# Performance work log

Hardware: AMD Instinct MI355X
Metric: run time of the kernel (lower is better)

The kernel has to match this reference:

```python
import jax, jax.numpy as jnp
import numpy as np

H, DH = 6, 64
D = H * DH
SQRT_DH = np.float32(np.sqrt(DH))


def _pool_norm(tok, ids):
    # masked mean pooling over tokens, then L2 normalize (Encoder.mean_pooling + normalize)
    mask = (ids > 0).astype(tok.dtype)[:, :, None]
    s = jnp.sum(tok * mask, axis=1) / jnp.clip(jnp.sum(mask, axis=1), 1e-9, None)
    return s / jnp.clip(jnp.linalg.norm(s, axis=1, keepdims=True), 1e-12, None)


def setup_inputs() -> dict:
    key = jax.random.key(0)
    ks = jax.random.split(key, 16)
    N_MSG, N_CON, L, E = 10000, 20000, 16, 128000
    s = 0.05
    eye = jnp.eye(DH, dtype=jnp.float32)
    inp = {}
    inp['tok_msg'] = jax.random.normal(ks[0], (N_MSG, L, D), jnp.float32)
    inp['tok_con'] = jax.random.normal(ks[1], (N_CON, L, D), jnp.float32)
    inp['ids_msg'] = jax.random.randint(ks[2], (N_MSG, L), 0, 100)
    inp['ids_con'] = jax.random.randint(ks[3], (N_CON, L), 0, 100)
    inp['src_cm'] = jax.random.randint(ks[4], (E,), 0, N_CON)
    inp['dst_cm'] = jax.random.randint(ks[5], (E,), 0, N_MSG)
    inp['src_mc'] = jax.random.randint(ks[6], (E,), 0, N_MSG)
    inp['dst_mc'] = jax.random.randint(ks[7], (E,), 0, N_CON)
    inp['lin_W'] = jax.random.normal(ks[8], (2, D, D), jnp.float32) * s
    inp['lin_b'] = jnp.zeros((2, D), jnp.float32)
    inp['kW'] = jax.random.normal(ks[9], (2, 2, D, D), jnp.float32) * s
    inp['kb'] = jnp.zeros((2, 2, D), jnp.float32)
    inp['qW'] = jax.random.normal(ks[10], (2, 2, D, D), jnp.float32) * s
    inp['qb'] = jnp.zeros((2, 2, D), jnp.float32)
    inp['vW'] = jax.random.normal(ks[11], (2, 2, D, D), jnp.float32) * s
    inp['vb'] = jnp.zeros((2, 2, D), jnp.float32)
    inp['aW'] = jax.random.normal(ks[12], (2, 2, D, D), jnp.float32) * s
    inp['ab'] = jnp.zeros((2, 2, D), jnp.float32)
    inp['a_rel'] = jax.random.normal(ks[13], (2, 2, H, DH, DH), jnp.float32) * s + eye
    inp['m_rel'] = jax.random.normal(ks[14], (2, 2, H, DH, DH), jnp.float32) * s + eye
    inp['p_rel'] = jnp.ones((2, 2, H), jnp.float32)
    inp['skip'] = jnp.ones((2, 2), jnp.float32)
    return inp


def _hgt_layer(xs, edges, kW, kb, qW, qb, vW, vb, aW, ab, a_rel, m_rel, p_rel, skip):
    # xs = [x_message, x_concept]; edges = ((src, dst) per edge type)
    k = [(xs[t] @ kW[t] + kb[t]).reshape(-1, H, DH) for t in (0, 1)]
    q = [(xs[t] @ qW[t] + qb[t]).reshape(-1, H, DH) for t in (0, 1)]
    v = [(xs[t] @ vW[t] + vb[t]).reshape(-1, H, DH) for t in (0, 1)]
    edge_meta = ((1, 0), (0, 1))  # edge type e -> (src_type, dst_type)
    agg = [None, None]
    for e, (s, d) in enumerate(edge_meta):
        si, di = edges[e]
        Nd = xs[d].shape[0]
        # relation-specific key/message transforms, per head: [E, H, DH]
        ke = jnp.einsum('ehd,hdf->ehf', k[s][si], a_rel[e])
        score = jnp.einsum('ehf,ehf->eh', q[d][di], ke) * p_rel[e] / SQRT_DH
        # softmax over incoming edges per destination node
        m = jax.ops.segment_max(score, di, num_segments=Nd)
        ex = jnp.exp(score - m[di])
        den = jax.ops.segment_sum(ex, di, num_segments=Nd)
        alpha = ex / den[di]
        msg = jnp.einsum('ehd,hdf->ehf', v[s][si], m_rel[e]) * alpha[:, :, None]
        agg[d] = jax.ops.segment_sum(msg, di, num_segments=Nd).reshape(Nd, D)
    out = []
    for t in (0, 1):
        o = jax.nn.gelu(agg[t], approximate=False) @ aW[t] + ab[t]
        a = jax.nn.sigmoid(skip[t])
        out.append(a * o + (1.0 - a) * xs[t])
    return out


def reference(tok_msg, tok_con, ids_msg, ids_con, src_cm, dst_cm, src_mc, dst_mc,
              lin_W, lin_b, kW, kb, qW, qb, vW, vb, aW, ab, a_rel, m_rel, p_rel, skip):
    x0 = jax.nn.relu(_pool_norm(tok_msg, ids_msg) @ lin_W[0] + lin_b[0])
    x1 = jax.nn.relu(_pool_norm(tok_con, ids_con) @ lin_W[1] + lin_b[1])
    edges = ((src_cm, dst_cm), (src_mc, dst_mc))
    xs = [x0, x1]
    for l in range(2):  # num_layers = 2 (hard-coded in MedicalEncoder)
        xs = _hgt_layer(xs, edges, kW[l], kb[l], qW[l], qb[l], vW[l], vb[l],
                        aW[l], ab[l], a_rel[l], m_rel[l], p_rel[l], skip[l])
    return xs[0]  # x_dict['message']
```

## Files before the change

kernel.cpp:

```cpp
#include <hip/hip_runtime.h>
#include <math.h>

#define H 6
#define DH 64
#define D 384
#define L 16
#define WSZ ((size_t)(D) * (D))
#define RSZ ((size_t)(H) * (DH) * (DH))

typedef __attribute__((ext_vector_type(8))) short short8;
typedef __attribute__((ext_vector_type(4))) float f32x4;
typedef unsigned int uint_;

__device__ __forceinline__ float bf2f(unsigned short u) {
  union { unsigned int i; float f; } x; x.i = ((unsigned int)u) << 16; return x.f;
}
__device__ __forceinline__ unsigned short f2bf(float f) {
  unsigned int x = __float_as_uint(f);
  x = x + 0x7fffu + ((x >> 16) & 1u);
  return (unsigned short)(x >> 16);
}
__device__ __forceinline__ float blo(unsigned int u) { return __uint_as_float(u << 16); }
__device__ __forceinline__ float bhi(unsigned int u) { return __uint_as_float(u & 0xffff0000u); }
__device__ __forceinline__ float geluf(float x) {
  return 0.5f * x * (1.0f + erff(x * 0.70710678118654752f));
}

__global__ void zero_int_kernel(int* p, long n) {
  long i = (long)blockIdx.x * blockDim.x + threadIdx.x;
  long stride = (long)gridDim.x * blockDim.x;
  for (; i < n; i += stride) p[i] = 0;
}

__global__ void pool_norm_kernel(const float* __restrict__ tokM, const int* __restrict__ idsM,
                                 unsigned short* __restrict__ outM, int NM,
                                 const float* __restrict__ tokC, const int* __restrict__ idsC,
                                 unsigned short* __restrict__ outC) {
  int n = blockIdx.x;
  const float* tok; const int* ids; unsigned short* out;
  if (n < NM) { tok = tokM; ids = idsM; out = outM; }
  else { n -= NM; tok = tokC; ids = idsC; out = outC; }
  int t = threadIdx.x;
  int rg = t / 96, c4 = t % 96;
  const float4* tp = (const float4*)(tok + (size_t)n * L * D);
  const int* ip = ids + (size_t)n * L;
  int cnt = 0;
#pragma unroll
  for (int l = 0; l < L; ++l) cnt += (ip[l] > 0);
  float4 s = {0.f, 0.f, 0.f, 0.f};
#pragma unroll
  for (int li = 0; li < 4; ++li) {
    int l = rg + li * 4;
    if (ip[l] > 0) {
      float4 v = tp[l * 96 + c4];
      s.x += v.x; s.y += v.y; s.z += v.z; s.w += v.w;
    }
  }
  __shared__ float4 part[4][96];
  part[rg][c4] = s;
  __syncthreads();
  float4 m4 = {0.f, 0.f, 0.f, 0.f};
  float dot = 0.f;
  float inv_cnt = 1.0f / fmaxf((float)cnt, 1e-9f);
  if (t < 96) {
    float4 a = part[0][t], b = part[1][t], c = part[2][t], d2 = part[3][t];
    m4.x = (a.x + b.x + c.x + d2.x) * inv_cnt;
    m4.y = (a.y + b.y + c.y + d2.y) * inv_cnt;
    m4.z = (a.z + b.z + c.z + d2.z) * inv_cnt;
    m4.w = (a.w + b.w + c.w + d2.w) * inv_cnt;
    dot = m4.x * m4.x + m4.y * m4.y + m4.z * m4.z + m4.w * m4.w;
  }
#pragma unroll
  for (int o = 32; o; o >>= 1) dot += __shfl_down(dot, o);
  __shared__ float wpart[6];
  if ((t & 63) == 0) wpart[t >> 6] = dot;
  __syncthreads();
  float tot = 0.f;
#pragma unroll
  for (int i = 0; i < 6; ++i) tot += wpart[i];
  float inv = 1.0f / fmaxf(sqrtf(tot), 1e-12f);
  if (t < 96) {
    uint2 o;
    o.x = (uint_)f2bf(m4.x * inv) | ((uint_)f2bf(m4.y * inv) << 16);
    o.y = (uint_)f2bf(m4.z * inv) | ((uint_)f2bf(m4.w * inv) << 16);
    ((uint2*)(out + (size_t)n * D))[t] = o;
  }
}

__global__ void prepw_kernel(const float* __restrict__ lin_W, const float* __restrict__ kW,
                             const float* __restrict__ qW, const float* __restrict__ vW,
                             const float* __restrict__ aW, const float* __restrict__ a_rel,
                             const float* __restrict__ m_rel, const float* __restrict__ p_rel,
                             const float* __restrict__ kb, const float* __restrict__ qb,
                             const float* __restrict__ vb,
                             unsigned short* __restrict__ wbuf, float* __restrict__ bbuf) {
  int z = blockIdx.z;
  int tx = threadIdx.x, ty = threadIdx.y;
  if (z == 14) {
    int i = (blockIdx.y * 12 + blockIdx.x) * 1024 + ty * 32 + tx;
    if (i >= 3456) return;
    int gemm, col;
    if (i < 1152) { gemm = 0; col = i; }
    else if (i < 2304) { gemm = 1; col = i - 1152; }
    else if (i < 2688) { gemm = 2; col = i - 2304; }
    else { gemm = 3; col = i - 2688; }
    int sec = col / D, j = col % D, h = j >> 6, r = j & 63;
    float out = 0.f;
    if (gemm == 0) {
      if (sec == 0) out = kb[j];
      else if (sec == 1) {
        const float* R = a_rel + (size_t)h * 4096 + (size_t)r * 64;
        float s = 0.f; for (int f = 0; f < 64; ++f) s += qb[h * 64 + f] * R[f];
        out = s * p_rel[h] * 0.125f;
      } else {
        const float* Mm = m_rel + RSZ + (size_t)h * 4096;
        float s = 0.f; for (int d = 0; d < 64; ++d) s += vb[h * 64 + d] * Mm[d * 64 + r]; out = s;
      }
    } else if (gemm == 1) {
      if (sec == 0) out = kb[D + j];
      else if (sec == 1) {
        const float* R = a_rel + RSZ + (size_t)h * 4096 + (size_t)r * 64;
        float s = 0.f; for (int f = 0; f < 64; ++f) s += qb[D + h * 64 + f] * R[f];
        out = s * p_rel[H + h] * 0.125f;
      } else {
        const float* Mm = m_rel + (size_t)h * 4096;
        float s = 0.f; for (int d = 0; d < 64; ++d) s += vb[D + h * 64 + d] * Mm[d * 64 + r]; out = s;
      }
    } else if (gemm == 2) {
      const float* R = a_rel + 2 * RSZ + (size_t)h * 4096 + (size_t)r * 64;
      float s = 0.f; for (int f = 0; f < 64; ++f) s += qb[2 * D + h * 64 + f] * R[f];
      out = s * p_rel[2 * H + h] * 0.125f;
    } else {
      if (sec == 0) out = kb[3 * D + j];
      else {
        const float* Mm = m_rel + 2 * RSZ + (size_t)h * 4096;
        float s = 0.f; for (int d = 0; d < 64; ++d) s += vb[3 * D + h * 64 + d] * Mm[d * 64 + r]; out = s;
      }
    }
    bbuf[i] = out;
    return;
  }
  const float* src; const float* rel = nullptr; const float* prl = nullptr; int type = 0;
  switch (z) {
    case 0: src = lin_W; break;
    case 1: src = lin_W + WSZ; break;
    case 2: src = kW; break;
    case 3: type = 1; src = qW; rel = a_rel; prl = p_rel; break;
    case 4: type = 2; src = vW; rel = m_rel + RSZ; break;
    case 5: src = kW + WSZ; break;
    case 6: type = 1; src = qW + WSZ; rel = a_rel + RSZ; prl = p_rel + H; break;
    case 7: type = 2; src = vW + WSZ; rel = m_rel; break;
    case 8: type = 1; src = qW + 2 * WSZ; rel = a_rel + 2 * RSZ; prl = p_rel + 2 * H; break;
    case 9: src = kW + 3 * WSZ; break;
    case 10: type = 2; src = vW + 3 * WSZ; rel = m_rel + 2 * RSZ; break;
    case 11: src = aW; break;
    case 12: src = aW + WSZ; break;
    default: src = aW + 2 * WSZ; break;
  }
  unsigned short* dst = wbuf + (size_t)z * WSZ;
  int bx = blockIdx.x * 32;
  int by = blockIdx.y * 32;
  if (type == 0) {
    __shared__ float tile[32][33];
    tile[ty][tx] = src[(size_t)(bx + ty) * D + by + tx];
    __syncthreads();
    dst[(size_t)(by + ty) * D + bx + tx] = f2bf(tile[tx][ty]);
  } else if (type == 1) {
    int h = by >> 6, d0 = by & 63;
    float sc = prl[h] * 0.125f;
    __shared__ float Wt_[32][65], Rt[32][65];
#pragma unroll
    for (int half = 0; half < 2; ++half) {
      Wt_[ty][tx + half * 32] = src[(size_t)(bx + ty) * D + h * 64 + tx + half * 32];
      Rt[ty][tx + half * 32] = rel[(size_t)h * 4096 + (size_t)(d0 + ty) * 64 + tx + half * 32];
    }
    __syncthreads();
    float s = 0.f;
#pragma unroll 16
    for (int f = 0; f < 64; ++f) s += Wt_[tx][f] * Rt[ty][f];
    dst[(size_t)(by + ty) * D + bx + tx] = f2bf(s * sc);
  } else {
    int h = by >> 6, f0 = by & 63;
    __shared__ float Wt_[32][65];
    __shared__ float Mt[64][33];
#pragma unroll
    for (int half = 0; half < 2; ++half) {
      Wt_[ty][tx + half * 32] = src[(size_t)(bx + ty) * D + h * 64 + tx + half * 32];
      Mt[ty * 2 + half][tx] = rel[(size_t)h * 4096 + (size_t)(ty * 2 + half) * 64 + f0 + tx];
    }
    __syncthreads();
    float s = 0.f;
#pragma unroll 16
    for (int d = 0; d < 64; ++d) s += Wt_[tx][d] * Mt[d][ty];
    dst[(size_t)(by + ty) * D + bx + tx] = f2bf(s);
  }
}

__global__ void count2_kernel(const int* __restrict__ d0, const int* __restrict__ d1,
                              int* __restrict__ deg0, int* __restrict__ deg1, int E) {
  int e = blockIdx.x * blockDim.x + threadIdx.x;
  if (e < E) atomicAdd(&deg0[d0[e]], 1);
  else if (e < 2 * E) atomicAdd(&deg1[d1[e - E]], 1);
}

__global__ void scan2_kernel(const int* __restrict__ deg0, int* __restrict__ off0, int N0,
                             const int* __restrict__ deg1, int* __restrict__ off1, int N1) {
  const int* deg = blockIdx.x ? deg1 : deg0;
  int* off = blockIdx.x ? off1 : off0;
  int N = blockIdx.x ? N1 : N0;
  __shared__ int wsum[16];
  __shared__ int carrySh;
  int tid = threadIdx.x;
  int lane = tid & 63, wid = tid >> 6;
  if (tid == 0) carrySh = 0;
  __syncthreads();
  for (int base = 0; base < N; base += 1024) {
    int i = base + tid;
    int v = (i < N) ? deg[i] : 0;
    int s = v;
#pragma unroll
    for (int o = 1; o < 64; o <<= 1) {
      int t = __shfl_up(s, o);
      if (lane >= o) s += t;
    }
    if (lane == 63) wsum[wid] = s;
    __syncthreads();
    int wpre = 0;
    for (int j = 0; j < wid; ++j) wpre += wsum[j];
    int c = carrySh;
    if (i < N) off[i] = c + wpre + s - v;
    __syncthreads();
    if (tid == 1023) carrySh = c + wpre + s;
    __syncthreads();
  }
  if (tid == 0) off[N] = carrySh;
}

__global__ void scatter2_kernel(const int* __restrict__ d0, const int* __restrict__ s0,
                                const int* __restrict__ off0, int* __restrict__ cur0,
                                int* __restrict__ el0,
                                const int* __restrict__ d1, const int* __restrict__ s1,
                                const int* __restrict__ off1, int* __restrict__ cur1,
                                int* __restrict__ el1, int E) {
  int e = blockIdx.x * blockDim.x + threadIdx.x;
  if (e < E) {
    int d = d0[e];
    el0[off0[d] + atomicAdd(&cur0[d], 1)] = s0[e];
  } else if (e < 2 * E) {
    int ee = e - E;
    int d = d1[ee];
    el1[off1[d] + atomicAdd(&cur1[d], 1)] = s1[ee];
  }
}

struct AttnP {
  const unsigned short* kb;
  const unsigned short* tqb;
  const unsigned short* vmb;
  const int* off;
  const int* elist;
  unsigned short* aggb;
  int N, sk, st, sv, nb;
};

__global__ void attn_kernel(AttnP a0, AttnP a1) {
  bool first = (int)blockIdx.x < a0.nb;
  AttnP a = first ? a0 : a1;
  int bx = first ? (int)blockIdx.x : (int)blockIdx.x - a0.nb;
  int node = bx * 4 + (threadIdx.x >> 6);
  int lane = threadIdx.x & 63;
  if (node >= a.N) return;
  int e0 = a.off[node], e1 = a.off[node + 1];
  const uint_* tq32 = (const uint_*)(a.tqb + (size_t)node * a.st);
  float tq0[3], tq1[3], m[3], den[3], ac0[3], ac1[3];
#pragma unroll
  for (int j = 0; j < 3; ++j) {
    uint_ u = tq32[lane + 64 * j];
    tq0[j] = blo(u); tq1[j] = bhi(u);
    m[j] = -1e30f; den[j] = 0.f; ac0[j] = 0.f; ac1[j] = 0.f;
  }
  int i = e0;
  for (; i + 2 <= e1; i += 2) {
    int s0 = a.elist[i], s1 = a.elist[i + 1];
    const uint_* k0 = (const uint_*)(a.kb + (size_t)s0 * a.sk);
    const uint_* k1 = (const uint_*)(a.kb + (size_t)s1 * a.sk);
    const uint_* v0 = (const uint_*)(a.vmb + (size_t)s0 * a.sv);
    const uint_* v1 = (const uint_*)(a.vmb + (size_t)s1 * a.sv);
    float pa[3], pb[3]; uint_ va[3], vb[3];
#pragma unroll
    for (int j = 0; j < 3; ++j) {
      uint_ ka = k0[lane + 64 * j], kbu = k1[lane + 64 * j];
      va[j] = v0[lane + 64 * j]; vb[j] = v1[lane + 64 * j];
      pa[j] = blo(ka) * tq0[j] + bhi(ka) * tq1[j];
      pb[j] = blo(kbu) * tq0[j] + bhi(kbu) * tq1[j];
    }
#pragma unroll
    for (int o = 1; o <= 16; o <<= 1)
#pragma unroll
      for (int j = 0; j < 3; ++j) {
        pa[j] += __shfl_xor(pa[j], o);
        pb[j] += __shfl_xor(pb[j], o);
      }
#pragma unroll
    for (int j = 0; j < 3; ++j) {
      float mn = fmaxf(m[j], fmaxf(pa[j], pb[j]));
      float r = __expf(m[j] - mn);
      float p0 = __expf(pa[j] - mn);
      float p1 = __expf(pb[j] - mn);
      den[j] = den[j] * r + p0 + p1;
      ac0[j] = ac0[j] * r + p0 * blo(va[j]) + p1 * blo(vb[j]);
      ac1[j] = ac1[j] * r + p0 * bhi(va[j]) + p1 * bhi(vb[j]);
      m[j] = mn;
    }
  }
  if (i < e1) {
    int s0 = a.elist[i];
    const uint_* k0 = (const uint_*)(a.kb + (size_t)s0 * a.sk);
    const uint_* v0 = (const uint_*)(a.vmb + (size_t)s0 * a.sv);
    float pa[3]; uint_ va[3];
#pragma unroll
    for (int j = 0; j < 3; ++j) {
      uint_ ka = k0[lane + 64 * j];
      va[j] = v0[lane + 64 * j];
      pa[j] = blo(ka) * tq0[j] + bhi(ka) * tq1[j];
    }
#pragma unroll
    for (int o = 1; o <= 16; o <<= 1)
#pragma unroll
      for (int j = 0; j < 3; ++j) pa[j] += __shfl_xor(pa[j], o);
#pragma unroll
    for (int j = 0; j < 3; ++j) {
      float mn = fmaxf(m[j], pa[j]);
      float r = __expf(m[j] - mn);
      float p0 = __expf(pa[j] - mn);
      den[j] = den[j] * r + p0;
      ac0[j] = ac0[j] * r + p0 * blo(va[j]);
      ac1[j] = ac1[j] * r + p0 * bhi(va[j]);
      m[j] = mn;
    }
  }
  uint_* op32 = (uint_*)(a.aggb + (size_t)node * D);
#pragma unroll
  for (int j = 0; j < 3; ++j) {
    float o0 = (e1 > e0) ? ac0[j] / den[j] : 0.f;
    float o1 = (e1 > e0) ? ac1[j] / den[j] : 0.f;
    op32[lane + 64 * j] = (uint_)f2bf(geluf(o0)) | ((uint_)f2bf(geluf(o1)) << 16);
  }
}

struct GemmP {
  const unsigned short* A;
  const unsigned short* Wt;
  const float* bias;
  float* Cf;
  unsigned short* Cb;
  const float* xold;
  const float* skipPtr;
  int M, N, cpitch, relu;
};

__global__ __launch_bounds__(256) void gemm_bf16(GemmP q0, GemmP q1) {
  GemmP p = blockIdx.z ? q1 : q0;
  const int bm = blockIdx.x * 128, bn = blockIdx.y * 128;
  if (bm >= p.M || bn >= p.N) return;
  __shared__ __align__(16) unsigned short As[2][128 * 64];
  __shared__ __align__(16) unsigned short Bs[2][128 * 64];
  const int tid = threadIdx.x;
  const int w = tid >> 6, lane = tid & 63;

  auto stage = [&](int t, int buf) {
#pragma unroll
    for (int i = 0; i < 4; ++i) {
      int cid = (w * 4 + i) * 64 + lane;
      int row = cid >> 3;
      int cg = (cid & 7) ^ (row & 7);
      int grow = bm + row;
      if (grow >= p.M) grow = p.M - 1;
      const unsigned short* gp = p.A + (size_t)grow * D + t * 64 + cg * 8;
      __builtin_amdgcn_global_load_lds((const __attribute__((address_space(1))) void*)gp,
                                       (__attribute__((address_space(3))) void*)&As[buf][(w * 4 + i) * 512],
                                       16, 0, 0);
    }
#pragma unroll
    for (int i = 0; i < 4; ++i) {
      int cid = (w * 4 + i) * 64 + lane;
      int row = cid >> 3;
      int cg = (cid & 7) ^ (row & 7);
      const unsigned short* gp = p.Wt + (size_t)(bn + row) * D + t * 64 + cg * 8;
      __builtin_amdgcn_global_load_lds((const __attribute__((address_space(1))) void*)gp,
                                       (__attribute__((address_space(3))) void*)&Bs[buf][(w * 4 + i) * 512],
                                       16, 0, 0);
    }
  };

  stage(0, 0);
  __syncthreads();

  const int wr = w >> 1, wc = w & 1;
  const int la = lane & 15, hi = lane >> 4;
  f32x4 acc[4][4] = {};

  for (int t = 0; t < 6; ++t) {
    if (t < 5) stage(t + 1, (t + 1) & 1);
    const unsigned short* Ab = As[t & 1];
    const unsigned short* Bb = Bs[t & 1];
#pragma unroll
    for (int ks = 0; ks < 2; ++ks) {
      int c = ks * 4 + hi;
      short8 af[4], bfr[4];
#pragma unroll
      for (int mi = 0; mi < 4; ++mi) {
        int row = wr * 64 + mi * 16 + la;
        af[mi] = *(const short8*)&Ab[row * 64 + ((c ^ (row & 7)) * 8)];
      }
#pragma unroll
      for (int n = 0; n < 4; ++n) {
        int col = wc * 64 + n * 16 + la;
        bfr[n] = *(const short8*)&Bb[col * 64 + ((c ^ (col & 7)) * 8)];
      }
#pragma unroll
      for (int mi = 0; mi < 4; ++mi)
#pragma unroll
        for (int n = 0; n < 4; ++n)
          acc[mi][n] = __builtin_amdgcn_mfma_f32_16x16x32_bf16(af[mi], bfr[n], acc[mi][n], 0, 0, 0);
    }
    __syncthreads();
  }

  float sa = 0.f;
  if (p.xold) sa = 1.0f / (1.0f + __expf(-*p.skipPtr));
#pragma unroll
  for (int mi = 0; mi < 4; ++mi) {
#pragma unroll
    for (int n = 0; n < 4; ++n) {
#pragma unroll
      for (int r = 0; r < 4; ++r) {
        int row = bm + wr * 64 + mi * 16 + hi * 4 + r;
        int col = bn + wc * 64 + n * 16 + la;
        if (row >= p.M) continue;
        float v = acc[mi][n][r] + p.bias[col];
        if (p.relu) v = fmaxf(v, 0.f);
        if (p.xold) v = sa * v + (1.0f - sa) * p.xold[(size_t)row * D + col];
        if (p.Cf) p.Cf[(size_t)row * p.cpitch + col] = v;
        if (p.Cb) p.Cb[(size_t)row * p.cpitch + col] = f2bf(v);
      }
    }
  }
}

extern "C" void kernel_launch(void* const* d_in, const int* in_sizes, int n_in,
                              void* d_out, int out_size, void* d_ws, size_t ws_size,
                              hipStream_t stream) {
  const float* tok_msg = (const float*)d_in[0];
  const float* tok_con = (const float*)d_in[1];
  const int* ids_msg = (const int*)d_in[2];
  const int* ids_con = (const int*)d_in[3];
  const int* src_cm = (const int*)d_in[4];
  const int* dst_cm = (const int*)d_in[5];
  const int* src_mc = (const int*)d_in[6];
  const int* dst_mc = (const int*)d_in[7];
  const float* lin_W = (const float*)d_in[8];
  const float* lin_b = (const float*)d_in[9];
  const float* kW = (const float*)d_in[10];
  const float* kb = (const float*)d_in[11];
  const float* qW = (const float*)d_in[12];
  const float* qb = (const float*)d_in[13];
  const float* vW = (const float*)d_in[14];
  const float* vb = (const float*)d_in[15];
  const float* aW = (const float*)d_in[16];
  const float* ab = (const float*)d_in[17];
  const float* a_rel = (const float*)d_in[18];
  const float* m_rel = (const float*)d_in[19];
  const float* p_rel = (const float*)d_in[20];
  const float* skip = (const float*)d_in[21];

  const int NM = in_sizes[2] / L;
  const int NC = in_sizes[3] / L;
  const int E = in_sizes[4];

  char* wsb = (char*)d_ws;
  size_t woff = 0;
  auto alloc = [&](size_t bytes) {
    woff = (woff + 255) & ~(size_t)255;
    void* p = wsb + woff;
    woff += bytes;
    return p;
  };
  const size_t NMe = (size_t)NM * D, NCe = (size_t)NC * D;
  unsigned short* poolM = (unsigned short*)alloc(NMe * 2);
  unsigned short* poolC = (unsigned short*)alloc(NCe * 2);
  float* x0f = (float*)alloc(NMe * 4);
  float* x1f = (float*)alloc(NCe * 4);
  float* xn0f = (float*)alloc(NMe * 4);
  unsigned short* x0b = (unsigned short*)alloc(NMe * 2);
  unsigned short* x1b = (unsigned short*)alloc(NCe * 2);
  unsigned short* xn0b = (unsigned short*)alloc(NMe * 2);
  unsigned short* xn1b = (unsigned short*)alloc(NCe * 2);
  unsigned short* projM1 = (unsigned short*)alloc((size_t)NM * 1152 * 2);
  unsigned short* projC1 = (unsigned short*)alloc((size_t)NC * 1152 * 2);
  unsigned short* projM2 = (unsigned short*)alloc((size_t)NM * 384 * 2);
  unsigned short* projC2 = (unsigned short*)alloc((size_t)NC * 768 * 2);
  unsigned short* aggM = (unsigned short*)alloc(NMe * 2);
  unsigned short* aggC = (unsigned short*)alloc(NCe * 2);
  unsigned short* wbuf = (unsigned short*)alloc(14 * WSZ * 2);
  float* bbuf = (float*)alloc(3456 * 4);
  long nz = 2L * NM + 2L * NC;
  int* ibase = (int*)alloc((size_t)(nz + NM + 1 + NC + 1 + 2L * E) * 4);
  int* deg0 = ibase;
  int* cur0 = deg0 + NM;
  int* deg1 = cur0 + NM;
  int* cur1 = deg1 + NC;
  int* off0 = cur1 + NC;
  int* off1 = off0 + NM + 1;
  int* el0 = off1 + NC + 1;
  int* el1 = el0 + E;

  dim3 b256(256);
  const int mbM = (NM + 127) / 128, mbC = (NC + 127) / 128;
  const int mbMax = (mbM > mbC) ? mbM : mbC;

  prepw_kernel<<<dim3(12, 12, 15), dim3(32, 32), 0, stream>>>(lin_W, kW, qW, vW, aW, a_rel,
                                                              m_rel, p_rel, kb, qb, vb, wbuf, bbuf);

  zero_int_kernel<<<64, b256, 0, stream>>>(ibase, nz);
  int eg2 = (2 * E + 255) / 256;
  count2_kernel<<<eg2, b256, 0, stream>>>(dst_cm, dst_mc, deg0, deg1, E);
  scan2_kernel<<<2, 1024, 0, stream>>>(deg0, off0, NM, deg1, off1, NC);
  scatter2_kernel<<<eg2, b256, 0, stream>>>(dst_cm, src_cm, off0, cur0, el0,
                                            dst_mc, src_mc, off1, cur1, el1, E);

  pool_norm_kernel<<<NM + NC, D, 0, stream>>>(tok_msg, ids_msg, poolM, NM, tok_con, ids_con, poolC);

  {
    GemmP p0 = {poolM, wbuf, lin_b, x0f, x0b, nullptr, nullptr, NM, D, D, 1};
    GemmP p1 = {poolC, wbuf + WSZ, lin_b + D, x1f, x1b, nullptr, nullptr, NC, D, D, 1};
    gemm_bf16<<<dim3(mbMax, 3, 2), b256, 0, stream>>>(p0, p1);
  }
  {
    GemmP p0 = {x0b, wbuf + 2 * WSZ, bbuf, nullptr, projM1, nullptr, nullptr, NM, 1152, 1152, 0};
    GemmP p1 = {x1b, wbuf + 5 * WSZ, bbuf + 1152, nullptr, projC1, nullptr, nullptr, NC, 1152, 1152, 0};
    gemm_bf16<<<dim3(mbMax, 9, 2), b256, 0, stream>>>(p0, p1);
  }
  {
    AttnP a0 = {projC1, projM1 + 384, projC1 + 768, off0, el0, aggM, NM, 1152, 1152, 1152, (NM + 3) / 4};
    AttnP a1 = {projM1, projC1 + 384, projM1 + 768, off1, el1, aggC, NC, 1152, 1152, 1152, (NC + 3) / 4};
    attn_kernel<<<(NM + 3) / 4 + (NC + 3) / 4, b256, 0, stream>>>(a0, a1);
  }
  {
    GemmP p0 = {aggM, wbuf + 11 * WSZ, ab, xn0f, xn0b, x0f, skip + 0, NM, D, D, 0};
    GemmP p1 = {aggC, wbuf + 12 * WSZ, ab + D, nullptr, xn1b, x1f, skip + 1, NC, D, D, 0};
    gemm_bf16<<<dim3(mbMax, 3, 2), b256, 0, stream>>>(p0, p1);
  }
  {
    GemmP p0 = {xn0b, wbuf + 8 * WSZ, bbuf + 2304, nullptr, projM2, nullptr, nullptr, NM, 384, 384, 0};
    GemmP p1 = {xn1b, wbuf + 9 * WSZ, bbuf + 2688, nullptr, projC2, nullptr, nullptr, NC, 768, 768, 0};
    gemm_bf16<<<dim3(mbMax, 6, 2), b256, 0, stream>>>(p0, p1);
  }
  {
    AttnP a0 = {projC2, projM2, projC2 + 384, off0, el0, aggM, NM, 768, 384, 768, (NM + 3) / 4};
    AttnP a1 = a0;
    attn_kernel<<<(NM + 3) / 4, b256, 0, stream>>>(a0, a1);
  }
  {
    GemmP p0 = {aggM, wbuf + 13 * WSZ, ab + 2 * D, (float*)d_out, nullptr, xn0f, skip + 2, NM, D, D, 0};
    GemmP p1 = p0;
    gemm_bf16<<<dim3(mbM, 3, 1), b256, 0, stream>>>(p0, p1);
  }
}
```

Baseline: 686.6 us.

## Fuse graph CSR build into pool, prep and GEMM kernels; drop fp32 residual copies

Edge degree counting now runs inside the pooling kernel, and the prefix scan is merged with the weight-prep kernel. The CSR scatter runs as an extra z-slice of the first GEMM launch. Together these cut several small kernel launches and let the graph preprocessing overlap with real work. The fp32 copies of the residual activations are removed and the skip connection reads the bf16 copies instead, which reduces memory traffic but lowers residual precision.

```diff
diff --git a/kernel.cpp b/kernel.cpp
--- a/kernel.cpp
+++ b/kernel.cpp
@@ -32,10 +32,20 @@
   for (; i < n; i += stride) p[i] = 0;
 }
 
-__global__ void pool_norm_kernel(const float* __restrict__ tokM, const int* __restrict__ idsM,
-                                 unsigned short* __restrict__ outM, int NM,
-                                 const float* __restrict__ tokC, const int* __restrict__ idsC,
-                                 unsigned short* __restrict__ outC) {
+__global__ void pool_count_kernel(const float* __restrict__ tokM, const int* __restrict__ idsM,
+                                  unsigned short* __restrict__ outM, int NM,
+                                  const float* __restrict__ tokC, const int* __restrict__ idsC,
+                                  unsigned short* __restrict__ outC,
+                                  const int* __restrict__ dc0, const int* __restrict__ dc1,
+                                  int* __restrict__ deg0, int* __restrict__ deg1, int E, int CH) {
+  {
+    int base = blockIdx.x * CH;
+    int e = base + threadIdx.x;
+    if (threadIdx.x < CH && e < 2 * E) {
+      if (e < E) atomicAdd(&deg0[dc0[e]], 1);
+      else atomicAdd(&deg1[dc1[e - E]], 1);
+    }
+  }
   int n = blockIdx.x;
   const float* tok; const int* ids; unsigned short* out;
   if (n < NM) { tok = tokM; ids = idsM; out = outM; }
@@ -87,54 +97,92 @@
   }
 }
 
-__global__ void prepw_kernel(const float* __restrict__ lin_W, const float* __restrict__ kW,
-                             const float* __restrict__ qW, const float* __restrict__ vW,
-                             const float* __restrict__ aW, const float* __restrict__ a_rel,
-                             const float* __restrict__ m_rel, const float* __restrict__ p_rel,
-                             const float* __restrict__ kb, const float* __restrict__ qb,
-                             const float* __restrict__ vb,
-                             unsigned short* __restrict__ wbuf, float* __restrict__ bbuf) {
-  int z = blockIdx.z;
-  int tx = threadIdx.x, ty = threadIdx.y;
+__global__ void prepscan_kernel(const float* __restrict__ lin_W, const float* __restrict__ kW,
+                                const float* __restrict__ qW, const float* __restrict__ vW,
+                                const float* __restrict__ aW, const float* __restrict__ a_rel,
+                                const float* __restrict__ m_rel, const float* __restrict__ p_rel,
+                                const float* __restrict__ kb, const float* __restrict__ qb,
+                                const float* __restrict__ vb,
+                                unsigned short* __restrict__ wbuf, float* __restrict__ bbuf,
+                                const int* __restrict__ deg0, int* __restrict__ off0, int N0,
+                                const int* __restrict__ deg1, int* __restrict__ off1, int N1) {
+  int bxg = blockIdx.x;
+  int tid = threadIdx.x;
+  if (bxg < 2) {
+    const int* deg = bxg ? deg1 : deg0;
+    int* off = bxg ? off1 : off0;
+    int N = bxg ? N1 : N0;
+    __shared__ int wsum[16];
+    __shared__ int carrySh;
+    int lane = tid & 63, wid = tid >> 6;
+    if (tid == 0) carrySh = 0;
+    __syncthreads();
+    for (int base = 0; base < N; base += 1024) {
+      int i = base + tid;
+      int v = (i < N) ? deg[i] : 0;
+      int s = v;
+#pragma unroll
+      for (int o = 1; o < 64; o <<= 1) {
+        int t2 = __shfl_up(s, o);
+        if (lane >= o) s += t2;
+      }
+      if (lane == 63) wsum[wid] = s;
+      __syncthreads();
+      int wpre = 0;
+      for (int j = 0; j < wid; ++j) wpre += wsum[j];
+      int c = carrySh;
+      if (i < N) off[i] = c + wpre + s - v;
+      __syncthreads();
+      if (tid == 1023) carrySh = c + wpre + s;
+      __syncthreads();
+    }
+    if (tid == 0) off[N] = carrySh;
+    return;
+  }
+  int q = bxg - 2;
+  int z = q / 144;
+  int r = q % 144;
+  int px = r % 12, py = r / 12;
+  int tx = tid & 31, ty = tid >> 5;
   if (z == 14) {
-    int i = (blockIdx.y * 12 + blockIdx.x) * 1024 + ty * 32 + tx;
+    int i = (py * 12 + px) * 1024 + tid;
     if (i >= 3456) return;
     int gemm, col;
     if (i < 1152) { gemm = 0; col = i; }
     else if (i < 2304) { gemm = 1; col = i - 1152; }
     else if (i < 2688) { gemm = 2; col = i - 2304; }
     else { gemm = 3; col = i - 2688; }
-    int sec = col / D, j = col % D, h = j >> 6, r = j & 63;
+    int sec = col / D, j = col % D, h = j >> 6, rr = j & 63;
     float out = 0.f;
     if (gemm == 0) {
       if (sec == 0) out = kb[j];
       else if (sec == 1) {
-        const float* R = a_rel + (size_t)h * 4096 + (size_t)r * 64;
+        const float* R = a_rel + (size_t)h * 4096 + (size_t)rr * 64;
         float s = 0.f; for (int f = 0; f < 64; ++f) s += qb[h * 64 + f] * R[f];
         out = s * p_rel[h] * 0.125f;
       } else {
         const float* Mm = m_rel + RSZ + (size_t)h * 4096;
-        float s = 0.f; for (int d = 0; d < 64; ++d) s += vb[h * 64 + d] * Mm[d * 64 + r]; out = s;
+        float s = 0.f; for (int d = 0; d < 64; ++d) s += vb[h * 64 + d] * Mm[d * 64 + rr]; out = s;
       }
     } else if (gemm == 1) {
       if (sec == 0) out = kb[D + j];
       else if (sec == 1) {
-        const float* R = a_rel + RSZ + (size_t)h * 4096 + (size_t)r * 64;
+        const float* R = a_rel + RSZ + (size_t)h * 4096 + (size_t)rr * 64;
         float s = 0.f; for (int f = 0; f < 64; ++f) s += qb[D + h * 64 + f] * R[f];
         out = s * p_rel[H + h] * 0.125f;
       } else {
         const float* Mm = m_rel + (size_t)h * 4096;
-        float s = 0.f; for (int d = 0; d < 64; ++d) s += vb[D + h * 64 + d] * Mm[d * 64 + r]; out = s;
+        float s = 0.f; for (int d = 0; d < 64; ++d) s += vb[D + h * 64 + d] * Mm[d * 64 + rr]; out = s;
       }
     } else if (gemm == 2) {
-      const float* R = a_rel + 2 * RSZ + (size_t)h * 4096 + (size_t)r * 64;
+      const float* R = a_rel + 2 * RSZ + (size_t)h * 4096 + (size_t)rr * 64;
       float s = 0.f; for (int f = 0; f < 64; ++f) s += qb[2 * D + h * 64 + f] * R[f];
       out = s * p_rel[2 * H + h] * 0.125f;
     } else {
       if (sec == 0) out = kb[3 * D + j];
       else {
         const float* Mm = m_rel + 2 * RSZ + (size_t)h * 4096;
-        float s = 0.f; for (int d = 0; d < 64; ++d) s += vb[3 * D + h * 64 + d] * Mm[d * 64 + r]; out = s;
+        float s = 0.f; for (int d = 0; d < 64; ++d) s += vb[3 * D + h * 64 + d] * Mm[d * 64 + rr]; out = s;
       }
     }
     bbuf[i] = out;
@@ -158,8 +206,8 @@
     default: src = aW + 2 * WSZ; break;
   }
   unsigned short* dst = wbuf + (size_t)z * WSZ;
-  int bx = blockIdx.x * 32;
-  int by = blockIdx.y * 32;
+  int bx = px * 32;
+  int by = py * 32;
   if (type == 0) {
     __shared__ float tile[32][33];
     tile[ty][tx] = src[(size_t)(bx + ty) * D + by + tx];
@@ -181,75 +229,18 @@
     dst[(size_t)(by + ty) * D + bx + tx] = f2bf(s * sc);
   } else {
     int h = by >> 6, f0 = by & 63;
-    __shared__ float Wt_[32][65];
+    __shared__ float Wt2[32][65];
     __shared__ float Mt[64][33];
 #pragma unroll
     for (int half = 0; half < 2; ++half) {
-      Wt_[ty][tx + half * 32] = src[(size_t)(bx + ty) * D + h * 64 + tx + half * 32];
+      Wt2[ty][tx + half * 32] = src[(size_t)(bx + ty) * D + h * 64 + tx + half * 32];
       Mt[ty * 2 + half][tx] = rel[(size_t)h * 4096 + (size_t)(ty * 2 + half) * 64 + f0 + tx];
     }
     __syncthreads();
     float s = 0.f;
 #pragma unroll 16
-    for (int d = 0; d < 64; ++d) s += Wt_[tx][d] * Mt[d][ty];
+    for (int d = 0; d < 64; ++d) s += Wt2[tx][d] * Mt[d][ty];
     dst[(size_t)(by + ty) * D + bx + tx] = f2bf(s);
-  }
-}
-
-__global__ void count2_kernel(const int* __restrict__ d0, const int* __restrict__ d1,
-                              int* __restrict__ deg0, int* __restrict__ deg1, int E) {
-  int e = blockIdx.x * blockDim.x + threadIdx.x;
-  if (e < E) atomicAdd(&deg0[d0[e]], 1);
-  else if (e < 2 * E) atomicAdd(&deg1[d1[e - E]], 1);
-}
-
-__global__ void scan2_kernel(const int* __restrict__ deg0, int* __restrict__ off0, int N0,
-                             const int* __restrict__ deg1, int* __restrict__ off1, int N1) {
-  const int* deg = blockIdx.x ? deg1 : deg0;
-  int* off = blockIdx.x ? off1 : off0;
-  int N = blockIdx.x ? N1 : N0;
-  __shared__ int wsum[16];
-  __shared__ int carrySh;
-  int tid = threadIdx.x;
-  int lane = tid & 63, wid = tid >> 6;
-  if (tid == 0) carrySh = 0;
-  __syncthreads();
-  for (int base = 0; base < N; base += 1024) {
-    int i = base + tid;
-    int v = (i < N) ? deg[i] : 0;
-    int s = v;
-#pragma unroll
-    for (int o = 1; o < 64; o <<= 1) {
-      int t = __shfl_up(s, o);
-      if (lane >= o) s += t;
-    }
-    if (lane == 63) wsum[wid] = s;
-    __syncthreads();
-    int wpre = 0;
-    for (int j = 0; j < wid; ++j) wpre += wsum[j];
-    int c = carrySh;
-    if (i < N) off[i] = c + wpre + s - v;
-    __syncthreads();
-    if (tid == 1023) carrySh = c + wpre + s;
-    __syncthreads();
-  }
-  if (tid == 0) off[N] = carrySh;
-}
-
-__global__ void scatter2_kernel(const int* __restrict__ d0, const int* __restrict__ s0,
-                                const int* __restrict__ off0, int* __restrict__ cur0,
-                                int* __restrict__ el0,
-                                const int* __restrict__ d1, const int* __restrict__ s1,
-                                const int* __restrict__ off1, int* __restrict__ cur1,
-                                int* __restrict__ el1, int E) {
-  int e = blockIdx.x * blockDim.x + threadIdx.x;
-  if (e < E) {
-    int d = d0[e];
-    el0[off0[d] + atomicAdd(&cur0[d], 1)] = s0[e];
-  } else if (e < 2 * E) {
-    int ee = e - E;
-    int d = d1[ee];
-    el1[off1[d] + atomicAdd(&cur1[d], 1)] = s1[ee];
   }
 }
 
@@ -354,12 +345,34 @@
   const float* bias;
   float* Cf;
   unsigned short* Cb;
-  const float* xold;
+  const unsigned short* xold;
   const float* skipPtr;
   int M, N, cpitch, relu;
 };
-
-__global__ __launch_bounds__(256) void gemm_bf16(GemmP q0, GemmP q1) {
+struct ScatP {
+  const int *d0, *s0, *off0;
+  int *cur0, *el0;
+  const int *d1, *s1, *off1;
+  int *cur1, *el1;
+  int E;
+};
+
+__global__ __launch_bounds__(256) void gemm_bf16(GemmP q0, GemmP q1, ScatP sc) {
+  if (blockIdx.z == 2) {
+    int nb = gridDim.x * gridDim.y;
+    int flat = blockIdx.y * gridDim.x + blockIdx.x;
+    for (int e = flat * 256 + threadIdx.x; e < 2 * sc.E; e += nb * 256) {
+      if (e < sc.E) {
+        int d = sc.d0[e];
+        sc.el0[sc.off0[d] + atomicAdd(&sc.cur0[d], 1)] = sc.s0[e];
+      } else {
+        int ee = e - sc.E;
+        int d = sc.d1[ee];
+        sc.el1[sc.off1[d] + atomicAdd(&sc.cur1[d], 1)] = sc.s1[ee];
+      }
+    }
+    return;
+  }
   GemmP p = blockIdx.z ? q1 : q0;
   const int bm = blockIdx.x * 128, bn = blockIdx.y * 128;
   if (bm >= p.M || bn >= p.N) return;
@@ -440,7 +453,7 @@
         if (row >= p.M) continue;
         float v = acc[mi][n][r] + p.bias[col];
         if (p.relu) v = fmaxf(v, 0.f);
-        if (p.xold) v = sa * v + (1.0f - sa) * p.xold[(size_t)row * D + col];
+        if (p.xold) v = sa * v + (1.0f - sa) * bf2f(p.xold[(size_t)row * D + col]);
         if (p.Cf) p.Cf[(size_t)row * p.cpitch + col] = v;
         if (p.Cb) p.Cb[(size_t)row * p.cpitch + col] = f2bf(v);
       }
@@ -489,9 +502,6 @@
   const size_t NMe = (size_t)NM * D, NCe = (size_t)NC * D;
   unsigned short* poolM = (unsigned short*)alloc(NMe * 2);
   unsigned short* poolC = (unsigned short*)alloc(NCe * 2);
-  float* x0f = (float*)alloc(NMe * 4);
-  float* x1f = (float*)alloc(NCe * 4);
-  float* xn0f = (float*)alloc(NMe * 4);
   unsigned short* x0b = (unsigned short*)alloc(NMe * 2);
   unsigned short* x1b = (unsigned short*)alloc(NCe * 2);
   unsigned short* xn0b = (unsigned short*)alloc(NMe * 2);
@@ -518,28 +528,28 @@
   dim3 b256(256);
   const int mbM = (NM + 127) / 128, mbC = (NC + 127) / 128;
   const int mbMax = (mbM > mbC) ? mbM : mbC;
-
-  prepw_kernel<<<dim3(12, 12, 15), dim3(32, 32), 0, stream>>>(lin_W, kW, qW, vW, aW, a_rel,
-                                                              m_rel, p_rel, kb, qb, vb, wbuf, bbuf);
+  ScatP scNone = {};
+  ScatP scAll = {dst_cm, src_cm, off0, cur0, el0, dst_mc, src_mc, off1, cur1, el1, E};
 
   zero_int_kernel<<<64, b256, 0, stream>>>(ibase, nz);
-  int eg2 = (2 * E + 255) / 256;
-  count2_kernel<<<eg2, b256, 0, stream>>>(dst_cm, dst_mc, deg0, deg1, E);
-  scan2_kernel<<<2, 1024, 0, stream>>>(deg0, off0, NM, deg1, off1, NC);
-  scatter2_kernel<<<eg2, b256, 0, stream>>>(dst_cm, src_cm, off0, cur0, el0,
-                                            dst_mc, src_mc, off1, cur1, el1, E);
-
-  pool_norm_kernel<<<NM + NC, D, 0, stream>>>(tok_msg, ids_msg, poolM, NM, tok_con, ids_con, poolC);
-
-  {
-    GemmP p0 = {poolM, wbuf, lin_b, x0f, x0b, nullptr, nullptr, NM, D, D, 1};
-    GemmP p1 = {poolC, wbuf + WSZ, lin_b + D, x1f, x1b, nullptr, nullptr, NC, D, D, 1};
-    gemm_bf16<<<dim3(mbMax, 3, 2), b256, 0, stream>>>(p0, p1);
+
+  const int CH = (2 * E + (NM + NC) - 1) / (NM + NC);
+  pool_count_kernel<<<NM + NC, D, 0, stream>>>(tok_msg, ids_msg, poolM, NM, tok_con, ids_con, poolC,
+                                               dst_cm, dst_mc, deg0, deg1, E, CH);
+
+  prepscan_kernel<<<2 + 15 * 144, 1024, 0, stream>>>(lin_W, kW, qW, vW, aW, a_rel, m_rel, p_rel,
+                                                     kb, qb, vb, wbuf, bbuf,
+                                                     deg0, off0, NM, deg1, off1, NC);
+
+  {
+    GemmP p0 = {poolM, wbuf, lin_b, nullptr, x0b, nullptr, nullptr, NM, D, D, 1};
+    GemmP p1 = {poolC, wbuf + WSZ, lin_b + D, nullptr, x1b, nullptr, nullptr, NC, D, D, 1};
+    gemm_bf16<<<dim3(mbMax, 3, 3), b256, 0, stream>>>(p0, p1, scAll);
   }
   {
     GemmP p0 = {x0b, wbuf + 2 * WSZ, bbuf, nullptr, projM1, nullptr, nullptr, NM, 1152, 1152, 0};
     GemmP p1 = {x1b, wbuf + 5 * WSZ, bbuf + 1152, nullptr, projC1, nullptr, nullptr, NC, 1152, 1152, 0};
-    gemm_bf16<<<dim3(mbMax, 9, 2), b256, 0, stream>>>(p0, p1);
+    gemm_bf16<<<dim3(mbMax, 9, 2), b256, 0, stream>>>(p0, p1, scNone);
   }
   {
     AttnP a0 = {projC1, projM1 + 384, projC1 + 768, off0, el0, aggM, NM, 1152, 1152, 1152, (NM + 3) / 4};
@@ -547,14 +557,14 @@
     attn_kernel<<<(NM + 3) / 4 + (NC + 3) / 4, b256, 0, stream>>>(a0, a1);
   }
   {
-    GemmP p0 = {aggM, wbuf + 11 * WSZ, ab, xn0f, xn0b, x0f, skip + 0, NM, D, D, 0};
-    GemmP p1 = {aggC, wbuf + 12 * WSZ, ab + D, nullptr, xn1b, x1f, skip + 1, NC, D, D, 0};
-    gemm_bf16<<<dim3(mbMax, 3, 2), b256, 0, stream>>>(p0, p1);
+    GemmP p0 = {aggM, wbuf + 11 * WSZ, ab, nullptr, xn0b, x0b, skip + 0, NM, D, D, 0};
+    GemmP p1 = {aggC, wbuf + 12 * WSZ, ab + D, nullptr, xn1b, x1b, skip + 1, NC, D, D, 0};
+    gemm_bf16<<<dim3(mbMax, 3, 2), b256, 0, stream>>>(p0, p1, scNone);
   }
   {
     GemmP p0 = {xn0b, wbuf + 8 * WSZ, bbuf + 2304, nullptr, projM2, nullptr, nullptr, NM, 384, 384, 0};
     GemmP p1 = {xn1b, wbuf + 9 * WSZ, bbuf + 2688, nullptr, projC2, nullptr, nullptr, NC, 768, 768, 0};
-    gemm_bf16<<<dim3(mbMax, 6, 2), b256, 0, stream>>>(p0, p1);
+    gemm_bf16<<<dim3(mbMax, 6, 2), b256, 0, stream>>>(p0, p1, scNone);
   }
   {
     AttnP a0 = {projC2, projM2, projC2 + 384, off0, el0, aggM, NM, 768, 384, 768, (NM + 3) / 4};
@@ -562,8 +572,8 @@
     attn_kernel<<<(NM + 3) / 4, b256, 0, stream>>>(a0, a1);
   }
   {
-    GemmP p0 = {aggM, wbuf + 13 * WSZ, ab + 2 * D, (float*)d_out, nullptr, xn0f, skip + 2, NM, D, D, 0};
+    GemmP p0 = {aggM, wbuf + 13 * WSZ, ab + 2 * D, (float*)d_out, nullptr, xn0b, skip + 2, NM, D, D, 0};
     GemmP p1 = p0;
-    gemm_bf16<<<dim3(mbM, 3, 1), b256, 0, stream>>>(p0, p1);
-  }
-}
+    gemm_bf16<<<dim3(mbM, 3, 1), b256, 0, stream>>>(p0, p1, scNone);
+  }
+}
```

Result: faster. 610.0 us (-11.2%).
